# Optimization experiments

Measured on AMD Instinct MI355X. Metric: run time of the kernel, lower is better.

The kernel has to match this reference:

```python
import jax, jax.numpy as jnp
import numpy as np

N_NODES = 100000
N_EDGES = 1000000
IN_DIM = 64
HID = 64
N_CLUSTER = 30
REG = 0.01


def glorot(key, shape):
    lim = np.sqrt(6.0 / (shape[0] + shape[1]))
    return jax.random.uniform(key, shape, jnp.float32, -lim, lim)


def setup_inputs() -> dict:
    key = jax.random.key(0)
    k1, k2, k3, k4, k5 = jax.random.split(key, 5)
    x = jax.random.normal(k1, (N_NODES, IN_DIM), jnp.float32)
    edge_index = jax.random.randint(k2, (2, N_EDGES), 0, N_NODES, jnp.int64)
    edge_attr = jax.random.uniform(k3, (N_EDGES,), jnp.float32)
    W1 = glorot(k4, (IN_DIM, HID))
    b1 = jnp.zeros((HID,), jnp.float32)
    W2 = glorot(k5, (HID, N_CLUSTER))
    b2 = jnp.zeros((N_CLUSTER,), jnp.float32)
    return {"x": x, "edge_index": edge_index, "edge_attr": edge_attr,
            "W1": W1, "b1": b1, "W2": W2, "b2": b2}


def gcn_conv(x, W, b, src, dst, w):
    # PyG GCNConv with edge weights: add self-loops (weight 1), symmetric norm.
    h = x @ W  # [N, out]
    deg = jax.ops.segment_sum(w, dst, num_segments=N_NODES) + 1.0  # self-loop
    dinv = jax.lax.rsqrt(deg)
    norm = dinv[src] * w * dinv[dst]  # [E]
    agg = jax.ops.segment_sum(norm[:, None] * h[src], dst, num_segments=N_NODES)
    agg = agg + h / deg[:, None]  # self-loop contribution: norm = 1/deg
    return agg + b


def reference(x, edge_index, edge_attr, W1, b1, W2, b2):
    src, dst = edge_index[0], edge_index[1]
    h = jax.nn.relu(gcn_conv(x, W1, b1, src, dst, edge_attr))
    # dropout p=0 -> identity
    X2 = gcn_conv(h, W2, b2, src, dst, edge_attr)
    FX = jax.nn.softmax(X2, axis=-1)  # [N, C]
    FF = jnp.sum(FX[src] * FX[dst], axis=-1)  # [E]
    NFX = jnp.log(1.0 - FX ** 2)  # [N, C]
    preg = -jnp.sum(jnp.log(1.0001 - jnp.exp(jnp.sum(NFX, axis=0))))
    loss = jnp.mean((FF - edge_attr) ** 2)
    return FX, loss + REG * preg
```

## Files before the change

kernel.cpp:

```cpp
#include <hip/hip_runtime.h>
#include <hip/hip_fp16.h>
#include <math.h>

#define N_NODES 100000
#define N_EDGES 1000000
#define IN_DIM 64
#define HID 64
#define NC 30
#define NCP 32
#define REG_C 0.01f

#define NTILES (N_NODES / 16)
#define NBUCK 391
#define EPB_A 2048
#define NBLK_A 489
#define GEMM_BLOCKS 512

typedef _Float16 half8 __attribute__((ext_vector_type(8)));
typedef _Float16 h16x4 __attribute__((ext_vector_type(4)));
typedef float f32x4 __attribute__((ext_vector_type(4)));
typedef float f32x2 __attribute__((ext_vector_type(2)));

__device__ __forceinline__ unsigned char enc_fp8(float v) {
    return (unsigned char)(__builtin_amdgcn_cvt_pk_fp8_f32(v, v, 0, false) & 0xFF);
}
__device__ __forceinline__ f32x4 dec_fp8x4(unsigned u) {
    f32x4 r;
    r[0] = __builtin_amdgcn_cvt_f32_fp8((int)u, 0);
    r[1] = __builtin_amdgcn_cvt_f32_fp8((int)u, 1);
    r[2] = __builtin_amdgcn_cvt_f32_fp8((int)u, 2);
    r[3] = __builtin_amdgcn_cvt_f32_fp8((int)u, 3);
    return r;
}
__device__ __forceinline__ float dot4_fp8(unsigned a, unsigned b) {
    float s = __builtin_amdgcn_cvt_f32_fp8((int)a, 0) * __builtin_amdgcn_cvt_f32_fp8((int)b, 0);
    s += __builtin_amdgcn_cvt_f32_fp8((int)a, 1) * __builtin_amdgcn_cvt_f32_fp8((int)b, 1);
    s += __builtin_amdgcn_cvt_f32_fp8((int)a, 2) * __builtin_amdgcn_cvt_f32_fp8((int)b, 2);
    s += __builtin_amdgcn_cvt_f32_fp8((int)a, 3) * __builtin_amdgcn_cvt_f32_fp8((int)b, 3);
    return s;
}

__global__ void hist_gemm(const int* __restrict__ dst, int* __restrict__ histT,
                          const float* __restrict__ X, const float* __restrict__ W,
                          unsigned char* __restrict__ H8) {
    if (blockIdx.x < NBLK_A) {
        __shared__ int cnt[NBUCK];
        for (int i = threadIdx.x; i < NBUCK; i += 256) cnt[i] = 0;
        __syncthreads();
        int e0 = blockIdx.x * EPB_A;
#pragma unroll
        for (int j = 0; j < 8; ++j) {
            int e = e0 + j * 256 + threadIdx.x;
            if (e < N_EDGES) atomicAdd(&cnt[dst[e] >> 8], 1);
        }
        __syncthreads();
        for (int b = threadIdx.x; b < NBUCK; b += 256)
            histT[b * NBLK_A + blockIdx.x] = cnt[b];
        return;
    }
    const int lane = threadIdx.x & 63;
    const int wave = threadIdx.x >> 6;
    const int qd = lane >> 4;
    const int l = lane & 15;
    half8 bfrag[2][4];
#pragma unroll
    for (int kb = 0; kb < 2; ++kb)
#pragma unroll
        for (int t = 0; t < 4; ++t)
#pragma unroll
            for (int j = 0; j < 8; ++j)
                bfrag[kb][t][j] = (_Float16)W[(kb * 32 + qd * 8 + j) * 64 + t * 16 + l];

    const int gb = blockIdx.x - NBLK_A;
    const int waveStride = GEMM_BLOCKS * 4;
    for (int ntile = gb * 4 + wave; ntile < NTILES; ntile += waveStride) {
        const int node0 = ntile * 16;
        const float* arow = X + (size_t)(node0 + l) * 64 + qd * 8;
        half8 af0, af1;
#pragma unroll
        for (int j = 0; j < 8; ++j) {
            af0[j] = (_Float16)arow[j];
            af1[j] = (_Float16)arow[32 + j];
        }
        f32x4 acc[4];
#pragma unroll
        for (int t = 0; t < 4; ++t) acc[t] = (f32x4){0.f, 0.f, 0.f, 0.f};
#pragma unroll
        for (int t = 0; t < 4; ++t) {
            acc[t] = __builtin_amdgcn_mfma_f32_16x16x32_f16(af0, bfrag[0][t], acc[t], 0, 0, 0);
            acc[t] = __builtin_amdgcn_mfma_f32_16x16x32_f16(af1, bfrag[1][t], acc[t], 0, 0, 0);
        }
#pragma unroll
        for (int t = 0; t < 4; ++t)
#pragma unroll
            for (int rr = 0; rr < 4; ++rr)
                H8[(size_t)(node0 + qd * 4 + rr) * 64 + t * 16 + l] = enc_fp8(acc[t][rr]);
    }
}

__global__ void scanA(int* __restrict__ histT, int* __restrict__ bucketTotal) {
    __shared__ int sc[256];
    int b = blockIdx.x, tid = threadIdx.x;
    int i0 = 2 * tid, i1 = 2 * tid + 1;
    int v0 = (i0 < NBLK_A) ? histT[b * NBLK_A + i0] : 0;
    int v1 = (i1 < NBLK_A) ? histT[b * NBLK_A + i1] : 0;
    int ps = v0 + v1;
    sc[tid] = ps;
    __syncthreads();
    for (int off = 1; off < 256; off <<= 1) {
        int t = (tid >= off) ? sc[tid - off] : 0;
        __syncthreads();
        sc[tid] += t;
        __syncthreads();
    }
    int excl = sc[tid] - ps;
    if (i0 < NBLK_A) histT[b * NBLK_A + i0] = excl;
    if (i1 < NBLK_A) histT[b * NBLK_A + i1] = excl + v0;
    if (tid == 255) bucketTotal[b] = sc[255];
}

__global__ void scatter_coarse(const int* __restrict__ src, const int* __restrict__ dst,
                               const float* __restrict__ w, const int* __restrict__ histT,
                               const int* __restrict__ bucketTotal, int* __restrict__ bucketBase,
                               int2* __restrict__ sw, unsigned char* __restrict__ dl) {
    __shared__ int cur[NBUCK];
    __shared__ int sc[256];
    int bl = blockIdx.x, tid = threadIdx.x;
    int i0 = 2 * tid, i1 = 2 * tid + 1;
    int v0 = (i0 < NBUCK) ? bucketTotal[i0] : 0;
    int v1 = (i1 < NBUCK) ? bucketTotal[i1] : 0;
    int ps = v0 + v1;
    sc[tid] = ps;
    __syncthreads();
    for (int off = 1; off < 256; off <<= 1) {
        int t = (tid >= off) ? sc[tid - off] : 0;
        __syncthreads();
        sc[tid] += t;
        __syncthreads();
    }
    int excl = sc[tid] - ps;
    if (i0 < NBUCK) cur[i0] = excl + histT[i0 * NBLK_A + bl];
    if (i1 < NBUCK) cur[i1] = excl + v0 + histT[i1 * NBLK_A + bl];
    if (bl == 0) {
        if (i0 < NBUCK) bucketBase[i0] = excl;
        if (i1 < NBUCK) bucketBase[i1] = excl + v0;
        if (tid == 0) bucketBase[NBUCK] = N_EDGES;
    }
    __syncthreads();
    int e0 = bl * EPB_A;
#pragma unroll
    for (int j = 0; j < 8; ++j) {
        int e = e0 + j * 256 + threadIdx.x;
        if (e < N_EDGES) {
            int d = dst[e];
            int pos = atomicAdd(&cur[d >> 8], 1);
            sw[pos] = make_int2(src[e], __float_as_int(w[e]));
            dl[pos] = (unsigned char)(d & 255);
        }
    }
}

__global__ void fused_bucket(const int2* __restrict__ sw, const unsigned char* __restrict__ dl,
                             const int* __restrict__ bucketBase, float* __restrict__ dinv,
                             float* __restrict__ invdeg, int* __restrict__ rowptr,
                             int2* __restrict__ edata2) {
    __shared__ int cnt[256];
    __shared__ float degf[256];
    __shared__ int sc[256];
    __shared__ float ldinv[256];
    __shared__ int cur[256];
    int b = blockIdx.x, tid = threadIdx.x;
    cnt[tid] = 0; degf[tid] = 0.f;
    __syncthreads();
    int p0 = bucketBase[b], p1 = bucketBase[b + 1];
    for (int p = p0 + tid; p < p1; p += 256) {
        int d = dl[p];
        atomicAdd(&cnt[d], 1);
        atomicAdd(&degf[d], __int_as_float(sw[p].y));
    }
    __syncthreads();
    int c = cnt[tid];
    sc[tid] = c;
    __syncthreads();
    for (int off = 1; off < 256; off <<= 1) {
        int t = (tid >= off) ? sc[tid - off] : 0;
        __syncthreads();
        sc[tid] += t;
        __syncthreads();
    }
    int node = b * 256 + tid;
    int row = p0 + sc[tid] - c;
    float dv = 0.f;
    if (node < N_NODES) {
        float d = degf[tid] + 1.0f;
        dv = rsqrtf(d);
        dinv[node] = dv;
        invdeg[node] = 1.0f / d;
        rowptr[node] = row;
    }
    ldinv[tid] = dv;
    cur[tid] = row;
    __syncthreads();
    for (int p = p0 + tid; p < p1; p += 256) {
        int d = dl[p];
        int2 r = sw[p];
        float nw = __int_as_float(r.y) * ldinv[d];
        int pos = atomicAdd(&cur[d], 1);
        edata2[pos] = make_int2(r.x, __float_as_int(nw));
    }
    if (b == 0 && tid == 0) rowptr[N_NODES] = N_EDGES;
}

__global__ void agg64_fused(const int* __restrict__ rowptr, const int2* __restrict__ edata2,
                            const unsigned char* __restrict__ H8, const float* __restrict__ dinv,
                            const float* __restrict__ invdeg,
                            const float* __restrict__ b1, _Float16* __restrict__ h2h) {
    const int node = blockIdx.x * 4 + (threadIdx.x >> 6);
    const int lane = threadIdx.x & 63;
    const int s = lane >> 4;
    const int q = lane & 15;
    int p = rowptr[node], end = rowptr[node + 1];
    float acc[4][4] = {};
    for (; p + 15 < end; p += 16) {
        int2 e[4];
#pragma unroll
        for (int g = 0; g < 4; ++g) e[g] = edata2[p + 4 * g + s];
        unsigned u[4];
        float dv[4];
#pragma unroll
        for (int g = 0; g < 4; ++g) {
            u[g] = *(const unsigned*)(H8 + ((unsigned)e[g].x << 6) + (q << 2));
            dv[g] = dinv[e[g].x];
        }
#pragma unroll
        for (int g = 0; g < 4; ++g) {
            float n = dv[g] * __int_as_float(e[g].y);
            f32x4 d = dec_fp8x4(u[g]);
#pragma unroll
            for (int j = 0; j < 4; ++j)
                acc[g][j] += n * d[j];
        }
    }
    {
        int r = end - p;
        int2 e[4];
#pragma unroll
        for (int g = 0; g < 4; ++g) {
            e[g] = make_int2(0, 0);
            if (4 * g + s < r) e[g] = edata2[p + 4 * g + s];
        }
        unsigned u[4];
        float dv[4];
#pragma unroll
        for (int g = 0; g < 4; ++g) {
            u[g] = *(const unsigned*)(H8 + ((unsigned)e[g].x << 6) + (q << 2));
            dv[g] = dinv[e[g].x];
        }
#pragma unroll
        for (int g = 0; g < 4; ++g) {
            float n = dv[g] * __int_as_float(e[g].y);
            f32x4 d = dec_fp8x4(u[g]);
#pragma unroll
            for (int j = 0; j < 4; ++j)
                acc[g][j] += n * d[j];
        }
    }
    float v[4];
#pragma unroll
    for (int j = 0; j < 4; ++j) {
        float t = (acc[0][j] + acc[1][j]) + (acc[2][j] + acc[3][j]);
        t += __shfl_xor(t, 16);
        t += __shfl_xor(t, 32);
        v[j] = t;
    }
    unsigned us = *(const unsigned*)(H8 + ((unsigned)node << 6) + (q << 2));
    float idg = invdeg[node];
    f32x4 bv = *(const f32x4*)(b1 + (q << 2));
    if (s == 0) {
        f32x4 ds = dec_fp8x4(us);
        h16x4 hv;
#pragma unroll
        for (int j = 0; j < 4; ++j) {
            float rj = v[j] + ds[j] * idg + bv[j];
            hv[j] = (_Float16)fmaxf(rj, 0.f);
        }
        *(h16x4*)(h2h + ((unsigned)node << 6) + (q << 2)) = hv;
    }
}

__global__ void linear30(const _Float16* __restrict__ H, const float* __restrict__ W2,
                         __half* __restrict__ HH16) {
    __shared__ float sW[64 * NC];
    __shared__ float sH[8 * 64];
    for (int i = threadIdx.x; i < 64 * NC; i += blockDim.x) sW[i] = W2[i];
    int node0 = blockIdx.x * 8;
    for (int i = threadIdx.x; i < 8 * 64; i += blockDim.x) {
        int n = node0 + (i >> 6);
        sH[i] = (n < N_NODES) ? (float)H[(size_t)n * 64 + (i & 63)] : 0.f;
    }
    __syncthreads();
    int ln = threadIdx.x >> 5;
    int c = threadIdx.x & 31;
    int node = node0 + ln;
    if (node < N_NODES) {
        float acc = 0.f;
        if (c < NC) {
#pragma unroll
            for (int k = 0; k < 64; ++k) acc += sH[ln * 64 + k] * sW[k * NC + c];
        }
        HH16[(size_t)node * NCP + c] = __float2half(acc);
    }
}

__global__ void agg30_softmax_colsum(const int* __restrict__ rowptr, const int2* __restrict__ edata2,
                                     const __half* __restrict__ HH16, const float* __restrict__ dinv,
                                     const float* __restrict__ invdeg,
                                     const float* __restrict__ b2, float* __restrict__ FX,
                                     unsigned char* __restrict__ FX8,
                                     float* __restrict__ colsum_part) {
    const int lane = threadIdx.x & 63;
    const int waveInBlock = threadIdx.x >> 6;
    const int n = lane >> 4;
    const int c2 = lane & 15;
    const bool activeC = (c2 < 15);
    const int node = (blockIdx.x * 4 + waveInBlock) * 4 + n;

    float bb0 = activeC ? b2[2 * c2] : 0.f;
    float bb1 = activeC ? b2[2 * c2 + 1] : 0.f;

    int p = rowptr[node], end = rowptr[node + 1];
    float a0[8], a1[8];
#pragma unroll
    for (int k = 0; k < 8; ++k) { a0[k] = 0.f; a1[k] = 0.f; }
    const __half* __restrict__ Hc = HH16 + (c2 << 1);
    for (; p + 7 < end; p += 8) {
        int2 e[8];
#pragma unroll
        for (int k = 0; k < 8; ++k) e[k] = edata2[p + k];
        unsigned h[8];
        float dv[8];
#pragma unroll
        for (int k = 0; k < 8; ++k) {
            h[k] = *(const unsigned*)(Hc + ((unsigned)e[k].x << 5));
            dv[k] = dinv[e[k].x];
        }
#pragma unroll
        for (int k = 0; k < 8; ++k) {
            float nw = dv[k] * __int_as_float(e[k].y);
            float2 hf = __half22float2(*(const __half2*)&h[k]);
            a0[k] += nw * hf.x;
            a1[k] += nw * hf.y;
        }
    }
    {
        int r = end - p;
        int2 e[8];
#pragma unroll
        for (int k = 0; k < 8; ++k) {
            e[k] = make_int2(0, 0);
            if (k < r) e[k] = edata2[p + k];
        }
        unsigned h[8];
        float dv[8];
#pragma unroll
        for (int k = 0; k < 8; ++k) {
            h[k] = *(const unsigned*)(Hc + ((unsigned)e[k].x << 5));
            dv[k] = dinv[e[k].x];
        }
#pragma unroll
        for (int k = 0; k < 8; ++k) {
            float nw = dv[k] * __int_as_float(e[k].y);
            float2 hf = __half22float2(*(const __half2*)&h[k]);
            a0[k] += nw * hf.x;
            a1[k] += nw * hf.y;
        }
    }
    float s0 = ((a0[0] + a0[1]) + (a0[2] + a0[3])) + ((a0[4] + a0[5]) + (a0[6] + a0[7]));
    float s1 = ((a1[0] + a1[1]) + (a1[2] + a1[3])) + ((a1[4] + a1[5]) + (a1[6] + a1[7]));
    unsigned hsu = *(const unsigned*)(Hc + ((unsigned)node << 5));
    float2 hs = __half22float2(*(const __half2*)&hsu);
    float idg = invdeg[node];
    float x0 = activeC ? (s0 + hs.x * idg + bb0) : -INFINITY;
    float x1 = activeC ? (s1 + hs.y * idg + bb1) : -INFINITY;
    float mx = fmaxf(x0, x1);
    mx = fmaxf(mx, __shfl_xor(mx, 1));
    mx = fmaxf(mx, __shfl_xor(mx, 2));
    mx = fmaxf(mx, __shfl_xor(mx, 4));
    mx = fmaxf(mx, __shfl_xor(mx, 8));
    float e0 = activeC ? expf(x0 - mx) : 0.f;
    float e1 = activeC ? expf(x1 - mx) : 0.f;
    float sum = e0 + e1;
    sum += __shfl_xor(sum, 1);
    sum += __shfl_xor(sum, 2);
    sum += __shfl_xor(sum, 4);
    sum += __shfl_xor(sum, 8);
    float fx0 = e0 / sum;
    float fx1 = e1 / sum;

    if (activeC) {
        *(f32x2*)(FX + (size_t)node * NC + 2 * c2) = (f32x2){fx0, fx1};
        unsigned short pk = (unsigned short)((unsigned)enc_fp8(fx0) | ((unsigned)enc_fp8(fx1) << 8));
        *(unsigned short*)(FX8 + ((unsigned)node << 5) + (c2 << 1)) = pk;
    } else {
        *(unsigned short*)(FX8 + ((unsigned)node << 5) + (c2 << 1)) = 0;
    }
    float lacc0 = activeC ? log1pf(-fx0 * fx0) : 0.f;
    float lacc1 = activeC ? log1pf(-fx1 * fx1) : 0.f;
    lacc0 += __shfl_xor(lacc0, 16); lacc0 += __shfl_xor(lacc0, 32);
    lacc1 += __shfl_xor(lacc1, 16); lacc1 += __shfl_xor(lacc1, 32);
    __shared__ float part[4][32];
    if (lane < 16) {
        part[waveInBlock][2 * c2] = lacc0;
        part[waveInBlock][2 * c2 + 1] = lacc1;
    }
    __syncthreads();
    if (threadIdx.x < NC) {
        float v = part[0][threadIdx.x] + part[1][threadIdx.x] +
                  part[2][threadIdx.x] + part[3][threadIdx.x];
        atomicAdd(&colsum_part[(blockIdx.x & 63) * 32 + threadIdx.x], v);
    }
}

__global__ void edge_loss_plain(const int* __restrict__ src, const int* __restrict__ dst,
                                const float* __restrict__ w,
                                const unsigned char* __restrict__ FX8,
                                float* __restrict__ mse_part) {
    int e = blockIdx.x * blockDim.x + threadIdx.x;
    float v = 0.f;
    if (e < N_EDGES) {
        int sn = src[e];
        int dn = dst[e];
        const uint4* rs = (const uint4*)(FX8 + (size_t)sn * NCP);
        const uint4* rd = (const uint4*)(FX8 + (size_t)dn * NCP);
        uint4 a0 = rs[0], a1 = rs[1];
        uint4 b0 = rd[0], b1 = rd[1];
        float ff = dot4_fp8(a0.x, b0.x) + dot4_fp8(a0.y, b0.y) +
                   dot4_fp8(a0.z, b0.z) + dot4_fp8(a0.w, b0.w) +
                   dot4_fp8(a1.x, b1.x) + dot4_fp8(a1.y, b1.y) +
                   dot4_fp8(a1.z, b1.z) + dot4_fp8(a1.w, b1.w);
        float diff = ff - w[e];
        v = diff * diff;
    }
    for (int off = 32; off > 0; off >>= 1) v += __shfl_down(v, off);
    __shared__ float ps[4];
    int lane = threadIdx.x & 63, wv = threadIdx.x >> 6;
    if (lane == 0) ps[wv] = v;
    __syncthreads();
    if (threadIdx.x == 0)
        atomicAdd(&mse_part[blockIdx.x & 63], ps[0] + ps[1] + ps[2] + ps[3]);
}

__global__ void finalize(const float* __restrict__ colsum_part, const float* __restrict__ mse_part,
                         float* __restrict__ out_loss) {
    int t = threadIdx.x;
    float m = mse_part[t];
    for (int off = 32; off > 0; off >>= 1) m += __shfl_down(m, off);
    float term = 0.f;
    if (t < NC) {
        float s = 0.f;
        for (int k = 0; k < 64; ++k) s += colsum_part[k * 32 + t];
        term = logf(1.0001f - expf(s));
    }
    for (int off = 32; off > 0; off >>= 1) term += __shfl_down(term, off);
    if (t == 0)
        out_loss[0] = m / (float)N_EDGES - REG_C * term;
}

extern "C" void kernel_launch(void* const* d_in, const int* in_sizes, int n_in,
                              void* d_out, int out_size, void* d_ws, size_t ws_size,
                              hipStream_t stream) {
    const float* x  = (const float*)d_in[0];
    const int*   ei = (const int*)d_in[1];
    const float* ea = (const float*)d_in[2];
    const float* W1 = (const float*)d_in[3];
    const float* b1 = (const float*)d_in[4];
    const float* W2 = (const float*)d_in[5];
    const float* b2 = (const float*)d_in[6];
    const int* srcI = ei;
    const int* dstI = ei + N_EDGES;

    float* FX   = (float*)d_out;
    float* loss = FX + (size_t)N_NODES * NC;

    float* ws = (float*)d_ws;
    float*         dinv   = ws;
    float*         invdeg = ws + 100000;
    unsigned char* h8     = (unsigned char*)(ws + 200000);
    _Float16*      h2h    = (_Float16*)(ws + 1800000);
    __half*        hh16   = (__half*)(ws + 5000000);
    unsigned char* fx8    = (unsigned char*)(ws + 6600000);
    float*         colsum_part = ws + 7400000;
    float*         mse_part    = ws + 7402048;
    int*           rowptr = (int*)(ws + 7402112);
    int*           histT  = (int*)(ws + 7502114);
    int*           bucketTotal = (int*)(ws + 7693314);
    int*           bucketBase  = (int*)(ws + 7693706);
    int2*          sw     = (int2*)(ws + 7694098);
    unsigned char* dl     = (unsigned char*)(ws + 9694098);
    int2*          edata2 = (int2*)(ws + 9944098);

    hipMemsetAsync(colsum_part, 0, (2048 + 64) * sizeof(float), stream);

    hist_gemm<<<NBLK_A + GEMM_BLOCKS, 256, 0, stream>>>(dstI, histT, x, W1, h8);
    scanA<<<NBUCK, 256, 0, stream>>>(histT, bucketTotal);
    scatter_coarse<<<NBLK_A, 256, 0, stream>>>(srcI, dstI, ea, histT, bucketTotal,
                                               bucketBase, sw, dl);
    fused_bucket<<<NBUCK, 256, 0, stream>>>(sw, dl, bucketBase, dinv, invdeg, rowptr, edata2);
    agg64_fused<<<N_NODES / 4, 256, 0, stream>>>(rowptr, edata2, h8, dinv, invdeg, b1, h2h);
    linear30<<<(N_NODES + 7) / 8, 256, 0, stream>>>(h2h, W2, hh16);
    agg30_softmax_colsum<<<N_NODES / 16, 256, 0, stream>>>(rowptr, edata2, hh16, dinv, invdeg,
                                                           b2, FX, fx8, colsum_part);
    edge_loss_plain<<<(N_EDGES + 255) / 256, 256, 0, stream>>>(srcI, dstI, ea, fx8, mse_part);
    finalize<<<1, 64, 0, stream>>>(colsum_part, mse_part, loss);
}
```

Measured before the change: 264.5 us.

## Prescale node features by dinv to drop per-edge dinv gathers

Folds the source-side dinv factor into the node feature tables (a new scale8 kernel for layer 1, and linear30 output for layer 2), so both aggregation kernels no longer gather dinv[src] per edge. Self-loop terms now use dinv[node] times the prescaled value, so invdeg is removed. The GEMM writes fp16 to an intermediate buffer that scale8 then reads to produce fp8, which adds a kernel launch and extra traffic. Precision shifts slightly because the scaling is applied before fp8 quantization.

```diff
diff --git a/kernel.cpp b/kernel.cpp
--- a/kernel.cpp
+++ b/kernel.cpp
@@ -42,7 +42,7 @@
 
 __global__ void hist_gemm(const int* __restrict__ dst, int* __restrict__ histT,
                           const float* __restrict__ X, const float* __restrict__ W,
-                          unsigned char* __restrict__ H8) {
+                          _Float16* __restrict__ h1h) {
     if (blockIdx.x < NBLK_A) {
         __shared__ int cnt[NBUCK];
         for (int i = threadIdx.x; i < NBUCK; i += 256) cnt[i] = 0;
@@ -94,7 +94,7 @@
         for (int t = 0; t < 4; ++t)
 #pragma unroll
             for (int rr = 0; rr < 4; ++rr)
-                H8[(size_t)(node0 + qd * 4 + rr) * 64 + t * 16 + l] = enc_fp8(acc[t][rr]);
+                h1h[(size_t)(node0 + qd * 4 + rr) * 64 + t * 16 + l] = (_Float16)acc[t][rr];
     }
 }
 
@@ -162,8 +162,7 @@
 
 __global__ void fused_bucket(const int2* __restrict__ sw, const unsigned char* __restrict__ dl,
                              const int* __restrict__ bucketBase, float* __restrict__ dinv,
-                             float* __restrict__ invdeg, int* __restrict__ rowptr,
-                             int2* __restrict__ edata2) {
+                             int* __restrict__ rowptr, int2* __restrict__ edata2) {
     __shared__ int cnt[256];
     __shared__ float degf[256];
     __shared__ int sc[256];
@@ -195,7 +194,6 @@
         float d = degf[tid] + 1.0f;
         dv = rsqrtf(d);
         dinv[node] = dv;
-        invdeg[node] = 1.0f / d;
         rowptr[node] = row;
     }
     ldinv[tid] = dv;
@@ -211,9 +209,19 @@
     if (b == 0 && tid == 0) rowptr[N_NODES] = N_EDGES;
 }
 
+__global__ void scale8(const _Float16* __restrict__ h1h, const float* __restrict__ dinv,
+                       unsigned char* __restrict__ H8) {
+    int idx = blockIdx.x * 256 + threadIdx.x;
+    int node = idx >> 4;
+    float dv = dinv[node];
+    h16x4 hv = *(const h16x4*)(h1h + (size_t)idx * 4);
+    unsigned u = __builtin_amdgcn_cvt_pk_fp8_f32((float)hv[0] * dv, (float)hv[1] * dv, 0, false);
+    u = __builtin_amdgcn_cvt_pk_fp8_f32((float)hv[2] * dv, (float)hv[3] * dv, u, true);
+    *(unsigned*)(H8 + (size_t)idx * 4) = u;
+}
+
 __global__ void agg64_fused(const int* __restrict__ rowptr, const int2* __restrict__ edata2,
                             const unsigned char* __restrict__ H8, const float* __restrict__ dinv,
-                            const float* __restrict__ invdeg,
                             const float* __restrict__ b1, _Float16* __restrict__ h2h) {
     const int node = blockIdx.x * 4 + (threadIdx.x >> 6);
     const int lane = threadIdx.x & 63;
@@ -226,15 +234,12 @@
 #pragma unroll
         for (int g = 0; g < 4; ++g) e[g] = edata2[p + 4 * g + s];
         unsigned u[4];
-        float dv[4];
+#pragma unroll
+        for (int g = 0; g < 4; ++g)
+            u[g] = *(const unsigned*)(H8 + ((unsigned)e[g].x << 6) + (q << 2));
 #pragma unroll
         for (int g = 0; g < 4; ++g) {
-            u[g] = *(const unsigned*)(H8 + ((unsigned)e[g].x << 6) + (q << 2));
-            dv[g] = dinv[e[g].x];
-        }
-#pragma unroll
-        for (int g = 0; g < 4; ++g) {
-            float n = dv[g] * __int_as_float(e[g].y);
+            float n = __int_as_float(e[g].y);
             f32x4 d = dec_fp8x4(u[g]);
 #pragma unroll
             for (int j = 0; j < 4; ++j)
@@ -250,15 +255,12 @@
             if (4 * g + s < r) e[g] = edata2[p + 4 * g + s];
         }
         unsigned u[4];
-        float dv[4];
+#pragma unroll
+        for (int g = 0; g < 4; ++g)
+            u[g] = *(const unsigned*)(H8 + ((unsigned)e[g].x << 6) + (q << 2));
 #pragma unroll
         for (int g = 0; g < 4; ++g) {
-            u[g] = *(const unsigned*)(H8 + ((unsigned)e[g].x << 6) + (q << 2));
-            dv[g] = dinv[e[g].x];
-        }
-#pragma unroll
-        for (int g = 0; g < 4; ++g) {
-            float n = dv[g] * __int_as_float(e[g].y);
+            float n = __int_as_float(e[g].y);
             f32x4 d = dec_fp8x4(u[g]);
 #pragma unroll
             for (int j = 0; j < 4; ++j)
@@ -274,14 +276,14 @@
         v[j] = t;
     }
     unsigned us = *(const unsigned*)(H8 + ((unsigned)node << 6) + (q << 2));
-    float idg = invdeg[node];
+    float dvn = dinv[node];
     f32x4 bv = *(const f32x4*)(b1 + (q << 2));
     if (s == 0) {
         f32x4 ds = dec_fp8x4(us);
         h16x4 hv;
 #pragma unroll
         for (int j = 0; j < 4; ++j) {
-            float rj = v[j] + ds[j] * idg + bv[j];
+            float rj = v[j] + ds[j] * dvn + bv[j];
             hv[j] = (_Float16)fmaxf(rj, 0.f);
         }
         *(h16x4*)(h2h + ((unsigned)node << 6) + (q << 2)) = hv;
@@ -289,7 +291,7 @@
 }
 
 __global__ void linear30(const _Float16* __restrict__ H, const float* __restrict__ W2,
-                         __half* __restrict__ HH16) {
+                         const float* __restrict__ dinv, __half* __restrict__ HH16) {
     __shared__ float sW[64 * NC];
     __shared__ float sH[8 * 64];
     for (int i = threadIdx.x; i < 64 * NC; i += blockDim.x) sW[i] = W2[i];
@@ -308,13 +310,12 @@
 #pragma unroll
             for (int k = 0; k < 64; ++k) acc += sH[ln * 64 + k] * sW[k * NC + c];
         }
-        HH16[(size_t)node * NCP + c] = __float2half(acc);
+        HH16[(size_t)node * NCP + c] = __float2half(acc * dinv[node]);
     }
 }
 
 __global__ void agg30_softmax_colsum(const int* __restrict__ rowptr, const int2* __restrict__ edata2,
                                      const __half* __restrict__ HH16, const float* __restrict__ dinv,
-                                     const float* __restrict__ invdeg,
                                      const float* __restrict__ b2, float* __restrict__ FX,
                                      unsigned char* __restrict__ FX8,
                                      float* __restrict__ colsum_part) {
@@ -338,15 +339,12 @@
 #pragma unroll
         for (int k = 0; k < 8; ++k) e[k] = edata2[p + k];
         unsigned h[8];
-        float dv[8];
+#pragma unroll
+        for (int k = 0; k < 8; ++k)
+            h[k] = *(const unsigned*)(Hc + ((unsigned)e[k].x << 5));
 #pragma unroll
         for (int k = 0; k < 8; ++k) {
-            h[k] = *(const unsigned*)(Hc + ((unsigned)e[k].x << 5));
-            dv[k] = dinv[e[k].x];
-        }
-#pragma unroll
-        for (int k = 0; k < 8; ++k) {
-            float nw = dv[k] * __int_as_float(e[k].y);
+            float nw = __int_as_float(e[k].y);
             float2 hf = __half22float2(*(const __half2*)&h[k]);
             a0[k] += nw * hf.x;
             a1[k] += nw * hf.y;
@@ -361,15 +359,12 @@
             if (k < r) e[k] = edata2[p + k];
         }
         unsigned h[8];
-        float dv[8];
+#pragma unroll
+        for (int k = 0; k < 8; ++k)
+            h[k] = *(const unsigned*)(Hc + ((unsigned)e[k].x << 5));
 #pragma unroll
         for (int k = 0; k < 8; ++k) {
-            h[k] = *(const unsigned*)(Hc + ((unsigned)e[k].x << 5));
-            dv[k] = dinv[e[k].x];
-        }
-#pragma unroll
-        for (int k = 0; k < 8; ++k) {
-            float nw = dv[k] * __int_as_float(e[k].y);
+            float nw = __int_as_float(e[k].y);
             float2 hf = __half22float2(*(const __half2*)&h[k]);
             a0[k] += nw * hf.x;
             a1[k] += nw * hf.y;
@@ -379,9 +374,9 @@
     float s1 = ((a1[0] + a1[1]) + (a1[2] + a1[3])) + ((a1[4] + a1[5]) + (a1[6] + a1[7]));
     unsigned hsu = *(const unsigned*)(Hc + ((unsigned)node << 5));
     float2 hs = __half22float2(*(const __half2*)&hsu);
-    float idg = invdeg[node];
-    float x0 = activeC ? (s0 + hs.x * idg + bb0) : -INFINITY;
-    float x1 = activeC ? (s1 + hs.y * idg + bb1) : -INFINITY;
+    float dvn = dinv[node];
+    float x0 = activeC ? (s0 + hs.x * dvn + bb0) : -INFINITY;
+    float x1 = activeC ? (s1 + hs.y * dvn + bb1) : -INFINITY;
     float mx = fmaxf(x0, x1);
     mx = fmaxf(mx, __shfl_xor(mx, 1));
     mx = fmaxf(mx, __shfl_xor(mx, 2));
@@ -484,31 +479,32 @@
 
     float* ws = (float*)d_ws;
     float*         dinv   = ws;
-    float*         invdeg = ws + 100000;
     unsigned char* h8     = (unsigned char*)(ws + 200000);
     _Float16*      h2h    = (_Float16*)(ws + 1800000);
+    _Float16*      h1h    = (_Float16*)(ws + 5000000);
     __half*        hh16   = (__half*)(ws + 5000000);
     unsigned char* fx8    = (unsigned char*)(ws + 6600000);
-    float*         colsum_part = ws + 7400000;
-    float*         mse_part    = ws + 7402048;
-    int*           rowptr = (int*)(ws + 7402112);
-    int*           histT  = (int*)(ws + 7502114);
-    int*           bucketTotal = (int*)(ws + 7693314);
-    int*           bucketBase  = (int*)(ws + 7693706);
-    int2*          sw     = (int2*)(ws + 7694098);
-    unsigned char* dl     = (unsigned char*)(ws + 9694098);
-    int2*          edata2 = (int2*)(ws + 9944098);
+    float*         colsum_part = ws + 8200000;
+    float*         mse_part    = ws + 8202048;
+    int*           rowptr = (int*)(ws + 8202112);
+    int*           histT  = (int*)(ws + 8302114);
+    int*           bucketTotal = (int*)(ws + 8493314);
+    int*           bucketBase  = (int*)(ws + 8493706);
+    int2*          sw     = (int2*)(ws + 8494098);
+    unsigned char* dl     = (unsigned char*)(ws + 10494098);
+    int2*          edata2 = (int2*)(ws + 10744098);
 
     hipMemsetAsync(colsum_part, 0, (2048 + 64) * sizeof(float), stream);
 
-    hist_gemm<<<NBLK_A + GEMM_BLOCKS, 256, 0, stream>>>(dstI, histT, x, W1, h8);
+    hist_gemm<<<NBLK_A + GEMM_BLOCKS, 256, 0, stream>>>(dstI, histT, x, W1, h1h);
     scanA<<<NBUCK, 256, 0, stream>>>(histT, bucketTotal);
     scatter_coarse<<<NBLK_A, 256, 0, stream>>>(srcI, dstI, ea, histT, bucketTotal,
                                                bucketBase, sw, dl);
-    fused_bucket<<<NBUCK, 256, 0, stream>>>(sw, dl, bucketBase, dinv, invdeg, rowptr, edata2);
-    agg64_fused<<<N_NODES / 4, 256, 0, stream>>>(rowptr, edata2, h8, dinv, invdeg, b1, h2h);
-    linear30<<<(N_NODES + 7) / 8, 256, 0, stream>>>(h2h, W2, hh16);
-    agg30_softmax_colsum<<<N_NODES / 16, 256, 0, stream>>>(rowptr, edata2, hh16, dinv, invdeg,
+    fused_bucket<<<NBUCK, 256, 0, stream>>>(sw, dl, bucketBase, dinv, rowptr, edata2);
+    scale8<<<N_NODES * 16 / 256, 256, 0, stream>>>(h1h, dinv, h8);
+    agg64_fused<<<N_NODES / 4, 256, 0, stream>>>(rowptr, edata2, h8, dinv, b1, h2h);
+    linear30<<<(N_NODES + 7) / 8, 256, 0, stream>>>(h2h, W2, dinv, hh16);
+    agg30_softmax_colsum<<<N_NODES / 16, 256, 0, stream>>>(rowptr, edata2, hh16, dinv,
                                                            b2, FX, fx8, colsum_part);
     edge_loss_plain<<<(N_EDGES + 255) / 256, 256, 0, stream>>>(srcI, dstI, ea, fx8, mse_part);
     finalize<<<1, 64, 0, stream>>>(colsum_part, mse_part, loss);
```

After: 263.9 us. About the same (-0.2%).
